# Kernel tuning notes

Hardware: AMD Instinct MI355X
Metric: run time of the kernel (lower is better)

The kernel has to match this reference:

```python
import jax, jax.numpy as jnp
import numpy as np

N_NODES = 20000
N_EDGES = 320000
N_RELS = 200
DESC_LEN = 16
DIM_G = 64
DIM_WORD = 300
DIM_HIDDEN = 256
H_DIR = DIM_HIDDEN // 2  # per-direction GRU hidden
N_CLASS = 2000
V_WORD = 30000
V_DESC = 30000
B, T = 4, 32


def setup_inputs() -> dict:
    key = jax.random.key(0)
    ks = jax.random.split(key, 24)
    inp = {}
    # index tensors (pad token is 0; generate tokens in [1, V) so all positions valid)
    inp['questions'] = jax.random.randint(ks[0], (B, T), 1, V_WORD)
    inp['node_descs'] = jax.random.randint(ks[1], (N_NODES, DESC_LEN), 1, V_DESC)
    inp['edge_src'] = jax.random.randint(ks[2], (N_EDGES,), 0, N_NODES)
    inp['edge_dst'] = jax.random.randint(ks[3], (N_EDGES,), 0, N_NODES)
    inp['edge_type'] = jax.random.randint(ks[4], (N_EDGES,), 0, N_RELS)
    # embeddings (normal with std 1/sqrt(dim) as in original init)
    inp['emb_word'] = jax.random.normal(ks[5], (V_WORD, DIM_WORD)) / np.sqrt(DIM_WORD)
    inp['emb_desc'] = jax.random.normal(ks[6], (V_DESC, DIM_G)) / np.sqrt(DIM_G)
    # BiGRU params (gates order r,z,n; concatenated along last dim)
    s = 0.1
    inp['Wx_f'] = jax.random.normal(ks[7], (DIM_WORD, 3 * H_DIR)) * s
    inp['Wh_f'] = jax.random.normal(ks[8], (H_DIR, 3 * H_DIR)) * s
    inp['bx_f'] = jnp.zeros((3 * H_DIR,))
    inp['bh_f'] = jnp.zeros((3 * H_DIR,))
    inp['Wx_b'] = jax.random.normal(ks[9], (DIM_WORD, 3 * H_DIR)) * s
    inp['Wh_b'] = jax.random.normal(ks[10], (H_DIR, 3 * H_DIR)) * s
    inp['bx_b'] = jnp.zeros((3 * H_DIR,))
    inp['bh_b'] = jnp.zeros((3 * H_DIR,))
    # lin_h_to_g (kaiming-ish scale)
    inp['W_hg'] = jax.random.normal(ks[11], (DIM_HIDDEN, DIM_G)) * np.sqrt(2.0 / DIM_HIDDEN)
    inp['b_hg'] = jnp.zeros((DIM_G,))
    # RGCN basis decomposition
    inp['bases'] = jax.random.normal(ks[12], (1, DIM_G, DIM_G)) * np.sqrt(1.0 / DIM_G)
    inp['w_comp'] = jax.random.normal(ks[13], (N_RELS, 1))
    inp['rgcn_bias'] = jnp.zeros((DIM_G,))
    # classifier
    inp['W1'] = jax.random.normal(ks[14], (DIM_G + DIM_HIDDEN, 1024)) * np.sqrt(2.0 / (DIM_G + DIM_HIDDEN))
    inp['b1'] = jnp.zeros((1024,))
    inp['W2'] = jax.random.normal(ks[15], (1024, N_CLASS)) * np.sqrt(2.0 / 1024)
    inp['b2'] = jnp.zeros((N_CLASS,))
    return inp


def _gru_last_hidden(x, mask, Wx, Wh, bx, bh):
    """Run a GRU over time; hidden only updates where mask is True.
    x: [B,T,D], mask: [B,T]. Returns final hidden [B,H]."""
    bsz = x.shape[0]
    h0 = jnp.zeros((bsz, Wh.shape[0]), x.dtype)
    gx_all = x @ Wx + bx  # [B,T,3H] precompute input gates

    def step(h, inputs):
        gx, mt = inputs  # [B,3H], [B]
        gh = h @ Wh + bh
        xr, xz, xn = jnp.split(gx, 3, axis=-1)
        hr, hz, hn = jnp.split(gh, 3, axis=-1)
        r = jax.nn.sigmoid(xr + hr)
        z = jax.nn.sigmoid(xz + hz)
        n = jnp.tanh(xn + r * hn)
        h_new = (1.0 - z) * n + z * h
        h = jnp.where(mt[:, None], h_new, h)
        return h, None

    hT, _ = jax.lax.scan(step, h0, (gx_all.transpose(1, 0, 2), mask.T))
    return hT


def _rel_graph_conv(h, edge_src, edge_dst, edge_type, bases, w_comp, bias):
    """Basis-decomposed RGCN layer (DGL RelGraphConv, norm=None, no self-loop).
    h: [B,N,G]. W_r = sum_k w_comp[r,k] * bases[k]."""
    n = h.shape[1]
    # project through each basis first: [B,N,K,O]
    hb = jnp.einsum('bng,kgo->bnko', h, bases)
    # per-edge message: gather src, combine with relation coefficients -> [B,E,O]
    msg = jnp.einsum('beko,ek->beo', hb[:, edge_src], w_comp[edge_type])
    # scatter-add to destination nodes
    agg = jax.vmap(lambda m: jax.ops.segment_sum(m, edge_dst, num_segments=n))(msg)
    return jax.nn.relu(agg + bias)


def reference(questions, node_descs, edge_src, edge_dst, edge_type,
              emb_word, emb_desc,
              Wx_f, Wh_f, bx_f, bh_f, Wx_b, Wh_b, bx_b, bh_b,
              W_hg, b_hg, bases, w_comp, rgcn_bias,
              W1, b1, W2, b2):
    # ---- question encoding (BiGRU over non-pad tokens; pad id = 0) ----
    mask = questions != 0  # [B,T]
    x = emb_word[questions]  # [B,T,Dw] (dropout is identity at eval)
    hf = _gru_last_hidden(x, mask, Wx_f, Wh_f, bx_f, bh_f)
    hb = _gru_last_hidden(x[:, ::-1], mask[:, ::-1], Wx_b, Wh_b, bx_b, bh_b)
    q_emb = jnp.concatenate([hf, hb], axis=-1)  # [B, dim_hidden]

    # ---- attention-weighted node features from descriptions ----
    desc_emb = emb_desc[node_descs]          # [N,L,G]
    q_g = q_emb @ W_hg + b_hg                # [B,G]
    attn1 = jax.nn.softmax(jnp.einsum('nlg,bg->bnl', desc_emb, q_g), axis=-1)
    node_feat = jnp.einsum('bnl,nlg->bng', attn1, desc_emb)  # [B,N,G]

    # ---- one RGCN hidden layer over the KB graph ----
    node_feat = _rel_graph_conv(node_feat, edge_src, edge_dst, edge_type,
                                bases, w_comp, rgcn_bias)

    # ---- attention pooling over nodes ----
    attn2 = jax.nn.softmax(jnp.einsum('bng,bg->bn', node_feat, q_g), axis=1)
    node_agg = jnp.einsum('bn,bng->bg', attn2, node_feat)    # [B,G]

    # ---- classifier ----
    feat = jnp.concatenate([node_agg, q_emb], axis=-1)       # [B, G+H]
    logits = jax.nn.relu(feat @ W1 + b1) @ W2 + b2           # [B, n_class]
    return logits
```

## Files before the change

### kernel.cpp

```cpp
#include <hip/hip_runtime.h>
#include <hip/hip_bf16.h>
#include <math.h>

typedef __hip_bfloat16 bf16;

#define NNODES 20000
#define NEDGES 320000
#define DLEN   16
#define G      64
#define DW     300
#define DH     256
#define HD     128
#define G3     384
#define NCLS   2000
#define NB     4
#define TT     32
#define A2BLK  1024
#define A2MID  64

#define NBLK_CVT  384
#define NBLK_GX2  1536
#define NBLK_HIST ((NEDGES + 255) / 256)

__device__ __forceinline__ float ld(const float* p, size_t i) { return p[i]; }
__device__ __forceinline__ float ld(const bf16* p, size_t i) { return __bfloat162float(p[i]); }
__device__ __forceinline__ void st(float* p, size_t i, float v) { p[i] = v; }
__device__ __forceinline__ void st(bf16* p, size_t i, float v) { p[i] = __float2bfloat16(v); }
__device__ __forceinline__ float relu(float x) { return (x < 0.f) ? 0.f : x; }

struct __align__(8) bf4 { bf16 x, y, z, w; };

#define OFF_FLAG  ((size_t)0)
#define OFF_GX    (OFF_FLAG + 4)
#define OFF_WHF   (OFF_GX   + 2*NB*TT*G3)
#define OFF_QEMB  (OFF_WHF  + 2*HD*G3)
#define OFF_QG    (OFF_QEMB + NB*DH)
#define OFF_NF    (OFF_QG   + NB*G)
#define OFF_HB    (OFF_NF   + (size_t)NB*NNODES*G)
#define OFF_PART  (OFF_HB   + (size_t)NB*NNODES*G)
#define OFF_PART2 (OFF_PART + (size_t)A2BLK*NB*66)
#define OFF_DEG   (OFF_PART2+ (size_t)A2MID*NB*66)
#define OFF_OFFS  (OFF_DEG  + NNODES)
#define OFF_CUR   (OFF_OFFS + NNODES + 8)
#define OFF_SSRC  (OFF_CUR  + NNODES)
#define OFF_SCO   (OFF_SSRC + NEDGES)
#define OFF_HID   (OFF_SCO  + NEDGES)

__global__ void k_init(const unsigned* probe, int* flag, int* deg) {
    int i = blockIdx.x * 256 + threadIdx.x;
    if (i < NNODES) deg[i] = 0;
    if (blockIdx.x == 0 && threadIdx.x < 64) {
        int cnt = 0;
        for (int k = threadIdx.x; k < 4096; k += 64) {
            unsigned lo = probe[k] & 0xFFFFu;
            unsigned e = (lo >> 7) & 0xFFu;
            cnt += (e >= 0x66u && e <= 0x7Eu) ? 1 : 0;
        }
#pragma unroll
        for (int off = 1; off < 64; off <<= 1) cnt += __shfl_xor(cnt, off, 64);
        if (threadIdx.x == 0) *flag = (2 * cnt > 4096) ? 1 : 0;
    }
}

template <typename T>
__device__ void cvt_body(int id, const void* Whf_, const void* Whb_, float* whf) {
    if (id >= 2 * HD * G3) return;
    int d = id / (HD * G3), r = id % (HD * G3);
    const T* W = (const T*)(d ? Whb_ : Whf_);
    whf[id] = ld(W, (size_t)r);
}

template <typename T>
__device__ void gx2_body(int bx2, const int* questions, const void* emb_word_,
                         const void* Wxf_, const void* bxf_,
                         const void* Wxb_, const void* bxb_, float* gx,
                         float* xs, float* psum) {
    int tid = threadIdx.x;
    int jt = bx2 % 6;
    int rid = bx2 / 6;
    int step = rid & 31;
    int b = (rid >> 5) & 3;
    int d = rid >> 7;
    int t = d ? (TT - 1 - step) : step;
    int tok = questions[b * TT + t];
    const T* row = (const T*)emb_word_ + (size_t)tok * DW;
    for (int k = tid; k < DW; k += 256) xs[k] = ld(row, (size_t)k);
    __syncthreads();
    int lane = tid & 63, phase = tid >> 6;
    int j = jt * 64 + lane;
    const T* Wx = (const T*)(d ? Wxb_ : Wxf_);
    float acc = 0.f;
    int k0 = phase * 75;
#pragma unroll 15
    for (int kk = 0; kk < 75; kk++) {
        int k = k0 + kk;
        acc += xs[k] * ld(Wx, (size_t)k * G3 + j);
    }
    psum[tid] = acc;
    __syncthreads();
    if (phase == 0) {
        const T* bx = (const T*)(d ? bxb_ : bxf_);
        float tot = ld(bx, (size_t)j)
                  + psum[lane] + psum[64 + lane] + psum[128 + lane] + psum[192 + lane];
        gx[(size_t)rid * G3 + j] = tot;
    }
}

__global__ void k_prep(const int* flag, const void* Whf, const void* Whb, float* whf,
                       const int* questions, const void* emb_word,
                       const void* Wxf, const void* bxf,
                       const void* Wxb, const void* bxb, float* gx,
                       const int* edge_dst, int* deg) {
    __shared__ float xs[DW];
    __shared__ float psum[256];
    int bx = blockIdx.x;
    int tid = threadIdx.x;
    if (bx < NBLK_CVT) {
        int id = bx * 256 + tid;
        if (*flag) cvt_body<bf16>(id, Whf, Whb, whf);
        else       cvt_body<float>(id, Whf, Whb, whf);
    } else if (bx < NBLK_CVT + NBLK_GX2) {
        int bx2 = bx - NBLK_CVT;
        if (*flag) gx2_body<bf16>(bx2, questions, emb_word, Wxf, bxf, Wxb, bxb, gx, xs, psum);
        else       gx2_body<float>(bx2, questions, emb_word, Wxf, bxf, Wxb, bxb, gx, xs, psum);
    } else {
        int e = (bx - NBLK_CVT - NBLK_GX2) * 256 + tid;
        if (e < NEDGES) atomicAdd(&deg[edge_dst[e]], 1);
    }
}

template <typename T>
__device__ void gru_body(const int* questions, const float* gx, const float* whf,
                         const void* bhf_, const void* bhb_, float* qemb,
                         float* hsm, float* ghs) {
    int tid = threadIdx.x;
    int d = blockIdx.x >> 2, b = blockIdx.x & 3;
    int half = tid / G3, j = tid - half * G3;
    const float* wh = whf + (size_t)d * HD * G3 + (size_t)half * 64 * G3 + j;
    float w[64];
#pragma unroll
    for (int m = 0; m < 64; m++) w[m] = wh[(size_t)m * G3];
    const T* bh = (const T*)(d ? bhb_ : bhf_);
    float bhj = (half == 0) ? ld(bh, (size_t)j) : 0.f;
    if (tid < HD) hsm[tid] = 0.f;
    const float* gxb = gx + ((size_t)(d * NB + b)) * TT * G3;
    __syncthreads();
    const float4* h4 = (const float4*)(hsm + half * 64);
    for (int step = 0; step < TT; step++) {
        float acc = bhj;
#pragma unroll
        for (int m4 = 0; m4 < 16; m4++) {
            float4 hp = h4[m4];
            acc = fmaf(hp.x, w[4 * m4 + 0], acc);
            acc = fmaf(hp.y, w[4 * m4 + 1], acc);
            acc = fmaf(hp.z, w[4 * m4 + 2], acc);
            acc = fmaf(hp.w, w[4 * m4 + 3], acc);
        }
        ghs[half * G3 + j] = acc;
        __syncthreads();
        if (tid < HD) {
            const float* gxp = gxb + step * G3;
            int t = d ? (TT - 1 - step) : step;
            bool msk = questions[b * TT + t] != 0;
            float gr = ghs[tid] + ghs[G3 + tid];
            float gz = ghs[HD + tid] + ghs[G3 + HD + tid];
            float gn = ghs[2 * HD + tid] + ghs[G3 + 2 * HD + tid];
            float r = 1.f / (1.f + expf(-(gxp[tid] + gr)));
            float z = 1.f / (1.f + expf(-(gxp[HD + tid] + gz)));
            float n = tanhf(gxp[2 * HD + tid] + r * gn);
            float hn = (1.f - z) * n + z * hsm[tid];
            if (msk) hsm[tid] = hn;
        }
        __syncthreads();
    }
    if (tid < HD) qemb[b * DH + d * HD + tid] = hsm[tid];
}
__global__ __launch_bounds__(2 * G3) void k_gru(const int* flag, const int* questions,
                                                const float* gx, const float* whf,
                                                const void* bhf, const void* bhb, float* qemb) {
    __shared__ __align__(16) float hsm[HD];
    __shared__ float ghs[2 * G3];
    if (*flag) gru_body<bf16>(questions, gx, whf, bhf, bhb, qemb, hsm, ghs);
    else       gru_body<float>(questions, gx, whf, bhf, bhb, qemb, hsm, ghs);
}

template <typename T>
__device__ void qg_body(const float* qemb, const void* W_hg_, const void* b_hg_, float* qg) {
    int tid = threadIdx.x;
    if (tid >= 256) return;
    int b = tid >> 6, g = tid & 63;
    const T* W = (const T*)W_hg_;
    float acc = ld((const T*)b_hg_, (size_t)g);
#pragma unroll 4
    for (int i = 0; i < DH; i++) acc += qemb[b * DH + i] * ld(W, (size_t)i * G + g);
    qg[b * G + g] = acc;
}

__global__ __launch_bounds__(1024) void k_scan_qg(const int* flag, const int* deg,
                                                  int* offs, int* cur,
                                                  const float* qemb, const void* W_hg,
                                                  const void* b_hg, float* qg) {
    if (blockIdx.x == 1) {
        if (*flag) qg_body<bf16>(qemb, W_hg, b_hg, qg);
        else       qg_body<float>(qemb, W_hg, b_hg, qg);
        return;
    }
    __shared__ int wtot[16];
    int t = threadIdx.x;
    int lane = t & 63, wave = t >> 6;
    int c[20];
    int base = t * 20;
    int run = 0;
#pragma unroll
    for (int i = 0; i < 20; i++) {
        int v = (base + i < NNODES) ? deg[base + i] : 0;
        c[i] = run;
        run += v;
    }
    int myrun = run;
    int inc = myrun;
#pragma unroll
    for (int off = 1; off < 64; off <<= 1) {
        int u = __shfl_up(inc, off, 64);
        if (lane >= off) inc += u;
    }
    if (lane == 63) wtot[wave] = inc;
    __syncthreads();
    if (t == 0) {
        int s = 0;
#pragma unroll
        for (int i = 0; i < 16; i++) { int v = wtot[i]; wtot[i] = s; s += v; }
        offs[NNODES] = s;
    }
    __syncthreads();
    int ebase = wtot[wave] + inc - myrun;
#pragma unroll
    for (int i = 0; i < 20; i++) {
        if (base + i < NNODES) {
            offs[base + i] = ebase + c[i];
            cur[base + i] = ebase + c[i];
        }
    }
}

template <typename T>
__device__ void scatter_body(const int* src, const int* dst, const int* typ,
                             const void* w_comp_, int* cur, int* ssrc, float* sco) {
    int e = blockIdx.x * 256 + threadIdx.x;
    if (e < NEDGES) {
        int dd = dst[e];
        int pos = atomicAdd(&cur[dd], 1);
        ssrc[pos] = src[e];
        sco[pos] = ld((const T*)w_comp_, (size_t)typ[e]);
    }
}
__global__ void k_scatter(const int* flag, const int* src, const int* dst, const int* typ,
                          const void* w_comp, int* cur, int* ssrc, float* sco) {
    if (*flag) scatter_body<bf16>(src, dst, typ, w_comp, cur, ssrc, sco);
    else       scatter_body<float>(src, dst, typ, w_comp, cur, ssrc, sco);
}

template <typename T>
__device__ void attn1_body(const int* node_descs, const void* emb_desc_,
                           const float* qg, bf16* nf16,
                           float* dsm, float* attn_s, float* qgs) {
    int tid = threadIdx.x;
    if (tid < NB * G) qgs[tid] = qg[tid];
    __syncthreads();
    const T* emb_desc = (const T*)emb_desc_;
    int w = tid >> 6, lane = tid & 63;
    int n = blockIdx.x * 4 + w;
    float dreg[DLEN];
    const int* nd = node_descs + n * DLEN;
    float* dw = dsm + (size_t)w * DLEN * 68;
#pragma unroll
    for (int l = 0; l < DLEN; l++) {
        int idx = nd[l];
        float v = ld(emb_desc, (size_t)idx * G + lane);
        dreg[l] = v;
        dw[l * 68 + lane] = v;
    }
    int lb = lane >> 4, ll = lane & 15;
    float acc = 0.f;
#pragma unroll
    for (int i = 0; i < 16; i++) {
        float4 a = *(const float4*)&dw[ll * 68 + 4 * i];
        float4 q = *(const float4*)&qgs[lb * G + 4 * i];
        acc = fmaf(a.x, q.x, acc);
        acc = fmaf(a.y, q.y, acc);
        acc = fmaf(a.z, q.z, acc);
        acc = fmaf(a.w, q.w, acc);
    }
    float mx = acc;
#pragma unroll
    for (int off = 1; off < 16; off <<= 1) mx = fmaxf(mx, __shfl_xor(mx, off, 64));
    float e = expf(acc - mx);
    float s = e;
#pragma unroll
    for (int off = 1; off < 16; off <<= 1) s += __shfl_xor(s, off, 64);
    attn_s[w * 64 + lane] = e / s;
#pragma unroll
    for (int b = 0; b < NB; b++) {
        float a = 0.f;
#pragma unroll
        for (int l = 0; l < DLEN; l++) a += attn_s[w * 64 + b * 16 + l] * dreg[l];
        nf16[((size_t)b * NNODES + n) * G + lane] = __float2bfloat16(a);
    }
}
__global__ __launch_bounds__(256) void k_attn1(const int* flag, const int* node_descs,
                                               const void* emb_desc, const float* qg, bf16* nf16) {
    __shared__ __align__(16) float dsm[4 * DLEN * 68];
    __shared__ float attn_s[4 * 64];
    __shared__ __align__(16) float qgs[NB * G];
    if (*flag) attn1_body<bf16>(node_descs, emb_desc, qg, nf16, dsm, attn_s, qgs);
    else       attn1_body<float>(node_descs, emb_desc, qg, nf16, dsm, attn_s, qgs);
}

template <typename T>
__device__ void hbg_body(const bf16* nf16, const void* bases_, bf16* hb16,
                         float* as, float* bs) {
    int tid = threadIdx.x;
    const T* bases = (const T*)bases_;
    for (int i = tid; i < G * G; i += 256) bs[(i >> 6) * 68 + (i & 63)] = ld(bases, (size_t)i);
    size_t r0 = (size_t)blockIdx.x * 64;
    const bf4* gA = (const bf4*)(nf16 + r0 * G);
#pragma unroll
    for (int i = 0; i < 4; i++) {
        int c = tid + i * 256;
        int row = c >> 4, col4 = c & 15;
        bf4 v = gA[c];
        float4 f;
        f.x = __bfloat162float(v.x);
        f.y = __bfloat162float(v.y);
        f.z = __bfloat162float(v.z);
        f.w = __bfloat162float(v.w);
        *(float4*)&as[row * 68 + col4 * 4] = f;
    }
    __syncthreads();
    int tx = tid & 15, ty = tid >> 4;
    float acc[4][4];
#pragma unroll
    for (int i = 0; i < 4; i++)
#pragma unroll
        for (int j = 0; j < 4; j++) acc[i][j] = 0.f;
#pragma unroll 4
    for (int g4 = 0; g4 < 16; g4++) {
        float4 b0 = *(const float4*)&bs[(4 * g4 + 0) * 68 + tx * 4];
        float4 b1 = *(const float4*)&bs[(4 * g4 + 1) * 68 + tx * 4];
        float4 b2 = *(const float4*)&bs[(4 * g4 + 2) * 68 + tx * 4];
        float4 b3 = *(const float4*)&bs[(4 * g4 + 3) * 68 + tx * 4];
#pragma unroll
        for (int i = 0; i < 4; i++) {
            float4 a = *(const float4*)&as[(ty * 4 + i) * 68 + g4 * 4];
            acc[i][0] = fmaf(a.x, b0.x, acc[i][0]);
            acc[i][0] = fmaf(a.y, b1.x, acc[i][0]);
            acc[i][0] = fmaf(a.z, b2.x, acc[i][0]);
            acc[i][0] = fmaf(a.w, b3.x, acc[i][0]);
            acc[i][1] = fmaf(a.x, b0.y, acc[i][1]);
            acc[i][1] = fmaf(a.y, b1.y, acc[i][1]);
            acc[i][1] = fmaf(a.z, b2.y, acc[i][1]);
            acc[i][1] = fmaf(a.w, b3.y, acc[i][1]);
            acc[i][2] = fmaf(a.x, b0.z, acc[i][2]);
            acc[i][2] = fmaf(a.y, b1.z, acc[i][2]);
            acc[i][2] = fmaf(a.z, b2.z, acc[i][2]);
            acc[i][2] = fmaf(a.w, b3.z, acc[i][2]);
            acc[i][3] = fmaf(a.x, b0.w, acc[i][3]);
            acc[i][3] = fmaf(a.y, b1.w, acc[i][3]);
            acc[i][3] = fmaf(a.z, b2.w, acc[i][3]);
            acc[i][3] = fmaf(a.w, b3.w, acc[i][3]);
        }
    }
#pragma unroll
    for (int i = 0; i < 4; i++) {
        size_t r = r0 + ty * 4 + i;
        int b = (int)(r / NNODES);
        int n = (int)(r - (size_t)b * NNODES);
        bf4 o;
        o.x = __float2bfloat16(acc[i][0]);
        o.y = __float2bfloat16(acc[i][1]);
        o.z = __float2bfloat16(acc[i][2]);
        o.w = __float2bfloat16(acc[i][3]);
        *(bf4*)&hb16[((size_t)n * NB + b) * G + tx * 4] = o;
    }
}
__global__ __launch_bounds__(256) void k_hbg(const int* flag, const bf16* nf16,
                                             const void* bases, bf16* hb16) {
    __shared__ __align__(16) float as[64 * 68];
    __shared__ __align__(16) float bs[64 * 68];
    if (*flag) hbg_body<bf16>(nf16, bases, hb16, as, bs);
    else       hbg_body<float>(nf16, bases, hb16, as, bs);
}

template <typename T>
__device__ void agg_body(const bf16* hb16, const int* offs, const int* ssrc,
                         const float* sco, const void* bias_, float* out_nf) {
    int tid = threadIdx.x;
    int b = tid >> 6, g = tid & 63;
    int dn = blockIdx.x;
    int s0 = offs[dn], s1 = offs[dn + 1];
    int boff = b * G + g;
    float acc = 0.f;
    int p = s0;
    for (; p + 15 < s1; p += 16) {
        int ix[16]; float co[16]; float x[16];
#pragma unroll
        for (int k = 0; k < 16; k++) { ix[k] = ssrc[p + k]; co[k] = sco[p + k]; }
#pragma unroll
        for (int k = 0; k < 16; k++) x[k] = __bfloat162float(hb16[(size_t)ix[k] * (NB * G) + boff]);
#pragma unroll
        for (int k = 0; k < 16; k++) acc += co[k] * x[k];
    }
    for (; p + 7 < s1; p += 8) {
        int ix[8]; float co[8]; float x[8];
#pragma unroll
        for (int k = 0; k < 8; k++) { ix[k] = ssrc[p + k]; co[k] = sco[p + k]; }
#pragma unroll
        for (int k = 0; k < 8; k++) x[k] = __bfloat162float(hb16[(size_t)ix[k] * (NB * G) + boff]);
#pragma unroll
        for (int k = 0; k < 8; k++) acc += co[k] * x[k];
    }
    for (; p + 3 < s1; p += 4) {
        int ix[4]; float co[4]; float x[4];
#pragma unroll
        for (int k = 0; k < 4; k++) { ix[k] = ssrc[p + k]; co[k] = sco[p + k]; }
#pragma unroll
        for (int k = 0; k < 4; k++) x[k] = __bfloat162float(hb16[(size_t)ix[k] * (NB * G) + boff]);
#pragma unroll
        for (int k = 0; k < 4; k++) acc += co[k] * x[k];
    }
    for (; p < s1; p++)
        acc += sco[p] * __bfloat162float(hb16[(size_t)ssrc[p] * (NB * G) + boff]);
    out_nf[((size_t)b * NNODES + dn) * G + g] = relu(acc + ld((const T*)bias_, (size_t)g));
}
__global__ __launch_bounds__(256) void k_agg(const int* flag, const bf16* hb16, const int* offs,
                                             const int* ssrc, const float* sco,
                                             const void* bias, float* out_nf) {
    if (*flag) agg_body<bf16>(hb16, offs, ssrc, sco, bias, out_nf);
    else       agg_body<float>(hb16, offs, ssrc, sco, bias, out_nf);
}

__device__ __forceinline__ void a2_update(float& M, float& L, float& A, float p, float v) {
    if (p > M) {
        float s = expf(M - p);
        A *= s; L *= s; M = p;
    }
    float e = expf(p - M);
    L += e;
    A = fmaf(e, v, A);
}

__global__ __launch_bounds__(256) void k_attn2(const float* rg, const float* qg, float* part) {
    int tid = threadIdx.x;
    int b = tid >> 6, lane = tid & 63;
    float q = qg[b * G + lane];
    int chunk = (NNODES + A2BLK - 1) / A2BLK;
    int n0 = blockIdx.x * chunk;
    int n1 = min(n0 + chunk, NNODES);
    const float* base = rg + (size_t)b * NNODES * G + lane;
    float M = -3.4e38f, L = 0.f, A = 0.f;
    int n = n0;
    for (; n + 3 < n1; n += 4) {
        float v0 = base[(size_t)(n + 0) * G];
        float v1 = base[(size_t)(n + 1) * G];
        float v2 = base[(size_t)(n + 2) * G];
        float v3 = base[(size_t)(n + 3) * G];
        float p0 = v0 * q, p1 = v1 * q, p2 = v2 * q, p3 = v3 * q;
#pragma unroll
        for (int off = 32; off >= 1; off >>= 1) {
            p0 += __shfl_xor(p0, off, 64);
            p1 += __shfl_xor(p1, off, 64);
            p2 += __shfl_xor(p2, off, 64);
            p3 += __shfl_xor(p3, off, 64);
        }
        a2_update(M, L, A, p0, v0);
        a2_update(M, L, A, p1, v1);
        a2_update(M, L, A, p2, v2);
        a2_update(M, L, A, p3, v3);
    }
    for (; n < n1; n++) {
        float v = base[(size_t)n * G];
        float p = v * q;
#pragma unroll
        for (int off = 32; off >= 1; off >>= 1) p += __shfl_xor(p, off, 64);
        a2_update(M, L, A, p, v);
    }
    float* pp = part + ((size_t)blockIdx.x * NB + b) * 66;
    if (lane == 0) { pp[0] = M; pp[1] = L; }
    pp[2 + lane] = A;
}

__global__ void k_attn2m(const float* part, float* part2) {
    int tid = threadIdx.x;
    int b = tid >> 6, lane = tid & 63;
    int grp = blockIdx.x;
    float M = -3.4e38f, L = 0.f, A = 0.f;
    for (int i = 0; i < A2BLK / A2MID; i++) {
        const float* pp = part + ((size_t)(grp * (A2BLK / A2MID) + i) * NB + b) * 66;
        float m = pp[0], l = pp[1], a = pp[2 + lane];
        float mn = fmaxf(M, m);
        float e1 = expf(M - mn), e2 = expf(m - mn);
        A = A * e1 + a * e2;
        L = L * e1 + l * e2;
        M = mn;
    }
    float* pq = part2 + ((size_t)grp * NB + b) * 66;
    if (lane == 0) { pq[0] = M; pq[1] = L; }
    pq[2 + lane] = A;
}

template <typename T>
__device__ void fc1_body(const float* part2, const float* qemb,
                         const void* W1_, const void* b1_, float* hid,
                         float* feat, float* psum) {
    int tid = threadIdx.x;
    int b = blockIdx.x >> 4, tile = blockIdx.x & 15;
    if (tid < 64) {
        float M = -3.4e38f, L = 0.f, A = 0.f;
        for (int p = 0; p < A2MID; p++) {
            const float* pp = part2 + ((size_t)p * NB + b) * 66;
            float m = pp[0], l = pp[1], a = pp[2 + tid];
            float mn = fmaxf(M, m);
            float e1 = expf(M - mn), e2 = expf(m - mn);
            A = A * e1 + a * e2;
            L = L * e1 + l * e2;
            M = mn;
        }
        feat[tid] = A / L;
        feat[tid + 256] = qemb[b * DH + tid + 192];
    } else {
        feat[tid] = qemb[b * DH + tid - G];
    }
    __syncthreads();
    int lane = tid & 63, phase = tid >> 6;
    int u = tile * 64 + lane;
    const T* W1 = (const T*)W1_;
    float acc = 0.f;
#pragma unroll 8
    for (int kk = 0; kk < 80; kk++) {
        int k = phase * 80 + kk;
        acc += feat[k] * ld(W1, (size_t)k * 1024 + u);
    }
    psum[tid] = acc;
    __syncthreads();
    if (phase == 0) {
        float tot = psum[lane] + psum[64 + lane] + psum[128 + lane] + psum[192 + lane]
                  + ld((const T*)b1_, (size_t)u);
        hid[b * 1024 + u] = relu(tot);
    }
}
__global__ __launch_bounds__(256) void k_fc1(const int* flag, const float* part2,
                                             const float* qemb, const void* W1, const void* b1,
                                             float* hid) {
    __shared__ float feat[320];
    __shared__ float psum[256];
    if (*flag) fc1_body<bf16>(part2, qemb, W1, b1, hid, feat, psum);
    else       fc1_body<float>(part2, qemb, W1, b1, hid, feat, psum);
}

template <typename T>
__device__ void fc2_body(const float* hid, const void* W2_, const void* b2_, void* out_,
                         float* hs, float* psum) {
    int tid = threadIdx.x;
    int b = blockIdx.x >> 5, tile = blockIdx.x & 31;
#pragma unroll
    for (int i = 0; i < 4; i++) hs[tid + 256 * i] = hid[b * 1024 + tid + 256 * i];
    __syncthreads();
    int lane = tid & 63, phase = tid >> 6;
    int c = tile * 64 + lane;
    bool ok = (c < NCLS);
    const T* W2 = (const T*)W2_;
    float acc = 0.f;
    if (ok) {
#pragma unroll 8
        for (int uu = 0; uu < 256; uu++) {
            int u = phase * 256 + uu;
            acc += hs[u] * ld(W2, (size_t)u * NCLS + c);
        }
    }
    psum[tid] = acc;
    __syncthreads();
    if (phase == 0 && ok) {
        float tot = psum[lane] + psum[64 + lane] + psum[128 + lane] + psum[192 + lane]
                  + ld((const T*)b2_, (size_t)c);
        st((T*)out_, (size_t)b * NCLS + c, tot);
    }
}
__global__ __launch_bounds__(256) void k_fc2(const int* flag, const float* hid,
                                             const void* W2, const void* b2v, void* out) {
    __shared__ float hs[1024];
    __shared__ float psum[256];
    if (*flag) fc2_body<bf16>(hid, W2, b2v, out, hs, psum);
    else       fc2_body<float>(hid, W2, b2v, out, hs, psum);
}

extern "C" void kernel_launch(void* const* d_in, const int* in_sizes, int n_in,
                              void* d_out, int out_size, void* d_ws, size_t ws_size,
                              hipStream_t stream) {
    const int* questions  = (const int*)d_in[0];
    const int* node_descs = (const int*)d_in[1];
    const int* edge_src   = (const int*)d_in[2];
    const int* edge_dst   = (const int*)d_in[3];
    const int* edge_type  = (const int*)d_in[4];
    const void* emb_word  = d_in[5];
    const void* emb_desc  = d_in[6];
    const void* Wx_f = d_in[7];
    const void* Wh_f = d_in[8];
    const void* bx_f = d_in[9];
    const void* bh_f = d_in[10];
    const void* Wx_b = d_in[11];
    const void* Wh_b = d_in[12];
    const void* bx_b = d_in[13];
    const void* bh_b = d_in[14];
    const void* W_hg = d_in[15];
    const void* b_hg = d_in[16];
    const void* bases = d_in[17];
    const void* w_comp = d_in[18];
    const void* rgcn_bias = d_in[19];
    const void* W1 = d_in[20];
    const void* b1 = d_in[21];
    const void* W2 = d_in[22];
    const void* b2 = d_in[23];

    float* ws = (float*)d_ws;
    int*      flag  = (int*)(ws + OFF_FLAG);
    float*    gx    = ws + OFF_GX;
    float*    whf   = ws + OFF_WHF;
    float*    qemb  = ws + OFF_QEMB;
    float*    qg    = ws + OFF_QG;
    float*    nf    = ws + OFF_NF;
    bf16*     nf16  = (bf16*)(ws + OFF_NF);
    bf16*     hb16  = (bf16*)(ws + OFF_HB);
    float*    part  = ws + OFF_PART;
    float*    part2 = ws + OFF_PART2;
    int*      deg   = (int*)(ws + OFF_DEG);
    int*      offs  = (int*)(ws + OFF_OFFS);
    int*      cur   = (int*)(ws + OFF_CUR);
    int*      ssrc  = (int*)(ws + OFF_SSRC);
    float*    sco   = ws + OFF_SCO;
    float*    hid   = ws + OFF_HID;

    hipLaunchKernelGGL(k_init, dim3(80), dim3(256), 0, stream,
                       (const unsigned*)emb_word, flag, deg);
    hipLaunchKernelGGL(k_prep, dim3(NBLK_CVT + NBLK_GX2 + NBLK_HIST), dim3(256), 0, stream,
                       flag, Wh_f, Wh_b, whf,
                       questions, emb_word, Wx_f, bx_f, Wx_b, bx_b, gx,
                       edge_dst, deg);
    hipLaunchKernelGGL(k_gru, dim3(8), dim3(2 * G3), 0, stream,
                       flag, questions, gx, whf, bh_f, bh_b, qemb);
    hipLaunchKernelGGL(k_scan_qg, dim3(2), dim3(1024), 0, stream,
                       flag, deg, offs, cur, qemb, W_hg, b_hg, qg);
    hipLaunchKernelGGL(k_scatter, dim3((NEDGES + 255) / 256), dim3(256), 0, stream,
                       flag, edge_src, edge_dst, edge_type, w_comp, cur, ssrc, sco);
    hipLaunchKernelGGL(k_attn1, dim3(NNODES / 4), dim3(256), 0, stream,
                       flag, node_descs, emb_desc, qg, nf16);
    hipLaunchKernelGGL(k_hbg, dim3(NB * NNODES / 64), dim3(256), 0, stream,
                       flag, nf16, bases, hb16);
    hipLaunchKernelGGL(k_agg, dim3(NNODES), dim3(256), 0, stream,
                       flag, hb16, offs, ssrc, sco, rgcn_bias, nf);
    hipLaunchKernelGGL(k_attn2, dim3(A2BLK), dim3(256), 0, stream, nf, qg, part);
    hipLaunchKernelGGL(k_attn2m, dim3(A2MID), dim3(256), 0, stream, part, part2);
    hipLaunchKernelGGL(k_fc1, dim3(NB * 16), dim3(256), 0, stream,
                       flag, part2, qemb, W1, b1, hid);
    hipLaunchKernelGGL(k_fc2, dim3(NB * 32), dim3(256), 0, stream,
                       flag, hid, W2, b2, d_out);
}
```

Baseline: 334.8 us.

## Co-schedule degree scan with GRU and fuse edge scatter with attn1

The CSR prefix scan moves into an extra block of the GRU kernel, so it runs alongside the serial GRU recurrence. The edge scatter and the description attention become one launch with block ranges split between the two tasks. The qg projection becomes its own small kernel. This removes one launch and lets independent stages overlap on idle CUs; the scan now uses 768 threads with 27 elements each, and the scan block's wtot array is sized for 12 waves.

After: 322.2 us. 1.04x faster.

```diff
diff --git a/kernel.cpp b/kernel.cpp
--- a/kernel.cpp
+++ b/kernel.cpp
@@ -21,6 +21,7 @@
 #define NBLK_CVT  384
 #define NBLK_GX2  1536
 #define NBLK_HIST ((NEDGES + 255) / 256)
+#define NBLK_SCAT ((NEDGES + 255) / 256)
 
 __device__ __forceinline__ float ld(const float* p, size_t i) { return p[i]; }
 __device__ __forceinline__ float ld(const bf16* p, size_t i) { return __bfloat162float(p[i]); }
@@ -175,19 +176,62 @@
     }
     if (tid < HD) qemb[b * DH + d * HD + tid] = hsm[tid];
 }
+
+__device__ void scan_body(const int* deg, int* offs, int* cur, int* wtot) {
+    int t = threadIdx.x;
+    int lane = t & 63, wave = t >> 6;
+    int c[27];
+    int base = t * 27;
+    int run = 0;
+#pragma unroll
+    for (int i = 0; i < 27; i++) {
+        int v = (base + i < NNODES) ? deg[base + i] : 0;
+        c[i] = run;
+        run += v;
+    }
+    int myrun = run, inc = run;
+#pragma unroll
+    for (int off = 1; off < 64; off <<= 1) {
+        int u = __shfl_up(inc, off, 64);
+        if (lane >= off) inc += u;
+    }
+    if (lane == 63) wtot[wave] = inc;
+    __syncthreads();
+    if (t == 0) {
+        int s = 0;
+#pragma unroll
+        for (int i = 0; i < 12; i++) { int v = wtot[i]; wtot[i] = s; s += v; }
+        offs[NNODES] = s;
+    }
+    __syncthreads();
+    int ebase = wtot[wave] + inc - myrun;
+#pragma unroll
+    for (int i = 0; i < 27; i++) {
+        if (base + i < NNODES) {
+            offs[base + i] = ebase + c[i];
+            cur[base + i] = ebase + c[i];
+        }
+    }
+}
+
 __global__ __launch_bounds__(2 * G3) void k_gru(const int* flag, const int* questions,
                                                 const float* gx, const float* whf,
-                                                const void* bhf, const void* bhb, float* qemb) {
+                                                const void* bhf, const void* bhb, float* qemb,
+                                                const int* deg, int* offs, int* cur) {
     __shared__ __align__(16) float hsm[HD];
     __shared__ float ghs[2 * G3];
-    if (*flag) gru_body<bf16>(questions, gx, whf, bhf, bhb, qemb, hsm, ghs);
-    else       gru_body<float>(questions, gx, whf, bhf, bhb, qemb, hsm, ghs);
+    __shared__ int wtot[12];
+    if (blockIdx.x < 8) {
+        if (*flag) gru_body<bf16>(questions, gx, whf, bhf, bhb, qemb, hsm, ghs);
+        else       gru_body<float>(questions, gx, whf, bhf, bhb, qemb, hsm, ghs);
+    } else {
+        scan_body(deg, offs, cur, wtot);
+    }
 }
 
 template <typename T>
 __device__ void qg_body(const float* qemb, const void* W_hg_, const void* b_hg_, float* qg) {
     int tid = threadIdx.x;
-    if (tid >= 256) return;
     int b = tid >> 6, g = tid & 63;
     const T* W = (const T*)W_hg_;
     float acc = ld((const T*)b_hg_, (size_t)g);
@@ -195,58 +239,15 @@
     for (int i = 0; i < DH; i++) acc += qemb[b * DH + i] * ld(W, (size_t)i * G + g);
     qg[b * G + g] = acc;
 }
-
-__global__ __launch_bounds__(1024) void k_scan_qg(const int* flag, const int* deg,
-                                                  int* offs, int* cur,
-                                                  const float* qemb, const void* W_hg,
-                                                  const void* b_hg, float* qg) {
-    if (blockIdx.x == 1) {
-        if (*flag) qg_body<bf16>(qemb, W_hg, b_hg, qg);
-        else       qg_body<float>(qemb, W_hg, b_hg, qg);
-        return;
-    }
-    __shared__ int wtot[16];
-    int t = threadIdx.x;
-    int lane = t & 63, wave = t >> 6;
-    int c[20];
-    int base = t * 20;
-    int run = 0;
-#pragma unroll
-    for (int i = 0; i < 20; i++) {
-        int v = (base + i < NNODES) ? deg[base + i] : 0;
-        c[i] = run;
-        run += v;
-    }
-    int myrun = run;
-    int inc = myrun;
-#pragma unroll
-    for (int off = 1; off < 64; off <<= 1) {
-        int u = __shfl_up(inc, off, 64);
-        if (lane >= off) inc += u;
-    }
-    if (lane == 63) wtot[wave] = inc;
-    __syncthreads();
-    if (t == 0) {
-        int s = 0;
-#pragma unroll
-        for (int i = 0; i < 16; i++) { int v = wtot[i]; wtot[i] = s; s += v; }
-        offs[NNODES] = s;
-    }
-    __syncthreads();
-    int ebase = wtot[wave] + inc - myrun;
-#pragma unroll
-    for (int i = 0; i < 20; i++) {
-        if (base + i < NNODES) {
-            offs[base + i] = ebase + c[i];
-            cur[base + i] = ebase + c[i];
-        }
-    }
-}
-
-template <typename T>
-__device__ void scatter_body(const int* src, const int* dst, const int* typ,
+__global__ void k_qg(const int* flag, const float* qemb, const void* W_hg,
+                     const void* b_hg, float* qg) {
+    if (*flag) qg_body<bf16>(qemb, W_hg, b_hg, qg);
+    else       qg_body<float>(qemb, W_hg, b_hg, qg);
+}
+
+template <typename T>
+__device__ void scatter_body(int e, const int* src, const int* dst, const int* typ,
                              const void* w_comp_, int* cur, int* ssrc, float* sco) {
-    int e = blockIdx.x * 256 + threadIdx.x;
     if (e < NEDGES) {
         int dd = dst[e];
         int pos = atomicAdd(&cur[dd], 1);
@@ -254,14 +255,9 @@
         sco[pos] = ld((const T*)w_comp_, (size_t)typ[e]);
     }
 }
-__global__ void k_scatter(const int* flag, const int* src, const int* dst, const int* typ,
-                          const void* w_comp, int* cur, int* ssrc, float* sco) {
-    if (*flag) scatter_body<bf16>(src, dst, typ, w_comp, cur, ssrc, sco);
-    else       scatter_body<float>(src, dst, typ, w_comp, cur, ssrc, sco);
-}
-
-template <typename T>
-__device__ void attn1_body(const int* node_descs, const void* emb_desc_,
+
+template <typename T>
+__device__ void attn1_body(int nb4, const int* node_descs, const void* emb_desc_,
                            const float* qg, bf16* nf16,
                            float* dsm, float* attn_s, float* qgs) {
     int tid = threadIdx.x;
@@ -269,7 +265,7 @@
     __syncthreads();
     const T* emb_desc = (const T*)emb_desc_;
     int w = tid >> 6, lane = tid & 63;
-    int n = blockIdx.x * 4 + w;
+    int n = nb4 * 4 + w;
     float dreg[DLEN];
     const int* nd = node_descs + n * DLEN;
     float* dw = dsm + (size_t)w * DLEN * 68;
@@ -307,13 +303,26 @@
         nf16[((size_t)b * NNODES + n) * G + lane] = __float2bfloat16(a);
     }
 }
-__global__ __launch_bounds__(256) void k_attn1(const int* flag, const int* node_descs,
-                                               const void* emb_desc, const float* qg, bf16* nf16) {
+
+__global__ __launch_bounds__(256) void k_sc_attn1(const int* flag,
+                                                  const int* src, const int* dst, const int* typ,
+                                                  const void* w_comp, int* cur,
+                                                  int* ssrc, float* sco,
+                                                  const int* node_descs, const void* emb_desc,
+                                                  const float* qg, bf16* nf16) {
     __shared__ __align__(16) float dsm[4 * DLEN * 68];
     __shared__ float attn_s[4 * 64];
     __shared__ __align__(16) float qgs[NB * G];
-    if (*flag) attn1_body<bf16>(node_descs, emb_desc, qg, nf16, dsm, attn_s, qgs);
-    else       attn1_body<float>(node_descs, emb_desc, qg, nf16, dsm, attn_s, qgs);
+    int bx = blockIdx.x;
+    if (bx < NBLK_SCAT) {
+        int e = bx * 256 + threadIdx.x;
+        if (*flag) scatter_body<bf16>(e, src, dst, typ, w_comp, cur, ssrc, sco);
+        else       scatter_body<float>(e, src, dst, typ, w_comp, cur, ssrc, sco);
+    } else {
+        int nb4 = bx - NBLK_SCAT;
+        if (*flag) attn1_body<bf16>(nb4, node_descs, emb_desc, qg, nf16, dsm, attn_s, qgs);
+        else       attn1_body<float>(nb4, node_descs, emb_desc, qg, nf16, dsm, attn_s, qgs);
+    }
 }
 
 template <typename T>
@@ -645,14 +654,12 @@
                        flag, Wh_f, Wh_b, whf,
                        questions, emb_word, Wx_f, bx_f, Wx_b, bx_b, gx,
                        edge_dst, deg);
-    hipLaunchKernelGGL(k_gru, dim3(8), dim3(2 * G3), 0, stream,
-                       flag, questions, gx, whf, bh_f, bh_b, qemb);
-    hipLaunchKernelGGL(k_scan_qg, dim3(2), dim3(1024), 0, stream,
-                       flag, deg, offs, cur, qemb, W_hg, b_hg, qg);
-    hipLaunchKernelGGL(k_scatter, dim3((NEDGES + 255) / 256), dim3(256), 0, stream,
-                       flag, edge_src, edge_dst, edge_type, w_comp, cur, ssrc, sco);
-    hipLaunchKernelGGL(k_attn1, dim3(NNODES / 4), dim3(256), 0, stream,
-                       flag, node_descs, emb_desc, qg, nf16);
+    hipLaunchKernelGGL(k_gru, dim3(9), dim3(2 * G3), 0, stream,
+                       flag, questions, gx, whf, bh_f, bh_b, qemb, deg, offs, cur);
+    hipLaunchKernelGGL(k_qg, dim3(1), dim3(256), 0, stream, flag, qemb, W_hg, b_hg, qg);
+    hipLaunchKernelGGL(k_sc_attn1, dim3(NBLK_SCAT + NNODES / 4), dim3(256), 0, stream,
+                       flag, edge_src, edge_dst, edge_type, w_comp, cur, ssrc, sco,
+                       node_descs, emb_desc, qg, nf16);
     hipLaunchKernelGGL(k_hbg, dim3(NB * NNODES / 64), dim3(256), 0, stream,
                        flag, nf16, bases, hb16);
     hipLaunchKernelGGL(k_agg, dim3(NNODES), dim3(256), 0, stream,
```
